# Optimization experiments

Measured on AMD Instinct MI355X. Metric: run time of the kernel, lower is better.

Reference implementation:

```python
import jax, jax.numpy as jnp
import numpy as np

N_HEADS = 16
ROPE_BASE = 10000.0


def _rope_cos_sin(seq_len, head_dim, dtype):
    half = head_dim // 2
    inv_freq = 1.0 / (ROPE_BASE ** (jnp.arange(0, half, dtype=jnp.float32) / half))
    ang = jnp.arange(seq_len, dtype=jnp.float32)[:, None] * inv_freq[None, :]  # [S, half]
    cos = jnp.concatenate([jnp.cos(ang), jnp.cos(ang)], axis=-1).astype(dtype)  # [S, hd]
    sin = jnp.concatenate([jnp.sin(ang), jnp.sin(ang)], axis=-1).astype(dtype)
    return cos, sin


def _rotate_half(x):
    half = x.shape[-1] // 2
    return jnp.concatenate([-x[..., half:], x[..., :half]], axis=-1)


def setup_inputs() -> dict:
    key = jax.random.key(0)
    k1, k2, k3 = jax.random.split(key, 3)
    B, S, D = 2, 2048, 1024
    x = jax.random.normal(k1, (B, S, D), dtype=jnp.float32)
    w_qkv = jax.random.normal(k2, (D, 3 * D), dtype=jnp.float32) * (1.0 / np.sqrt(D))
    w_out = jax.random.normal(k3, (D, D), dtype=jnp.float32) * (1.0 / np.sqrt(D))
    return {"x": x, "w_qkv": w_qkv, "w_out": w_out}


def reference(x, w_qkv, w_out):
    B, S, D = x.shape
    H = N_HEADS
    hd = D // H
    scale = 1.0 / np.sqrt(hd)

    qkv = x @ w_qkv  # [B, S, 3D]
    q, k, v = jnp.split(qkv, 3, axis=-1)
    # [B, H, S, hd]
    q = q.reshape(B, S, H, hd).transpose(0, 2, 1, 3)
    k = k.reshape(B, S, H, hd).transpose(0, 2, 1, 3)
    v = v.reshape(B, S, H, hd).transpose(0, 2, 1, 3)

    cos, sin = _rope_cos_sin(S, hd, x.dtype)  # [S, hd]
    q = q * cos + _rotate_half(q) * sin
    k = k * cos + _rotate_half(k) * sin

    scores = jnp.einsum("bhqd,bhkd->bhqk", q, k) * scale  # [B, H, S, S]
    causal = jnp.tril(jnp.ones((S, S), dtype=bool))
    scores = jnp.where(causal[None, None, :, :], scores, -jnp.inf)

    probs = jax.nn.softmax(scores.astype(jnp.float32), axis=-1).astype(q.dtype)
    out = jnp.einsum("bhqk,bhkd->bhqd", probs, v)  # [B, H, S, hd]
    out = out.transpose(0, 2, 1, 3).reshape(B, S, D)
    return out @ w_out
```

## Files before the change

### kernel.cpp

```cpp
#include <hip/hip_runtime.h>
#include <math.h>
#include <type_traits>

#define B_  2
#define S_  2048
#define D_  1024
#define H_  16

typedef short bf16x8 __attribute__((ext_vector_type(8)));
typedef short bf16x4 __attribute__((ext_vector_type(4)));
typedef float f32x4  __attribute__((ext_vector_type(4)));

__device__ __forceinline__ short f2bf(float f) {
    unsigned u = __builtin_bit_cast(unsigned, f);
    u += 0x7FFFu + ((u >> 16) & 1u);
    return (short)(u >> 16);
}
__device__ __forceinline__ float bf2f(short s) {
    unsigned u = ((unsigned)(unsigned short)s) << 16;
    return __builtin_bit_cast(float, u);
}

__device__ __forceinline__ void gload16(const short* g, const void* l) {
    __builtin_amdgcn_global_load_lds(
        (const __attribute__((address_space(1))) void*)g,
        (__attribute__((address_space(3))) void*)l, 16, 0, 0);
}

__device__ __forceinline__ void transpose_body(
    const float* __restrict__ in, short* __restrict__ out, int K, int N,
    int bx, int by, short (*t)[72], int tid)
{
    const int k0 = by * 64, n0 = bx * 64;
    const int r = tid >> 2;
    const int c = (tid & 3) * 16;
    const float* src = in + (size_t)(k0 + r) * N + n0 + c;
#pragma unroll
    for (int i = 0; i < 16; ++i) t[c + i][r] = f2bf(src[i]);
    __syncthreads();
    short* dst = out + (size_t)(n0 + r) * K + k0 + c;
    *(bf16x8*)(dst)     = *(const bf16x8*)&t[r][c];
    *(bf16x8*)(dst + 8) = *(const bf16x8*)&t[r][c + 8];
}

__global__ __launch_bounds__(256) void prep_kernel(
    const float* __restrict__ x, short* __restrict__ Xb,
    const float* __restrict__ w_qkv, short* __restrict__ Wqt,
    const float* __restrict__ w_out, short* __restrict__ Wot,
    float2* __restrict__ tab)
{
    __shared__ short t[64][72];
    const int bid = blockIdx.x;
    const int tid = threadIdx.x;
    if (bid < 2048) {
        int i = (bid * 256 + tid) * 8;
        float4 a = *(const float4*)(x + i);
        float4 b = *(const float4*)(x + i + 4);
        bf16x8 o;
        o[0] = f2bf(a.x); o[1] = f2bf(a.y); o[2] = f2bf(a.z); o[3] = f2bf(a.w);
        o[4] = f2bf(b.x); o[5] = f2bf(b.y); o[6] = f2bf(b.z); o[7] = f2bf(b.w);
        *(bf16x8*)(Xb + i) = o;
    } else if (bid < 2816) {
        int b2 = bid - 2048;
        transpose_body(w_qkv, Wqt, 1024, 3072, b2 % 48, b2 / 48, t, tid);
    } else if (bid < 3072) {
        int b2 = bid - 2816;
        transpose_body(w_out, Wot, 1024, 1024, b2 % 16, b2 / 16, t, tid);
    } else {
        int idx = (bid - 3072) * 256 + tid;
        int j = idx & 31, s = idx >> 5;
        float inv = powf(10000.0f, -(float)j * (1.0f / 32.0f));
        float sn, cs;
        sincosf((float)s * inv, &sn, &cs);
        tab[idx] = make_float2(cs, sn);
    }
}

__global__ __launch_bounds__(256) void gemm_bt_f32(
    const short* __restrict__ A, const short* __restrict__ Bt,
    float* __restrict__ C, int M, int N, int K)
{
    __shared__ short smem[18432];

    const int tid  = threadIdx.x;
    const int wave = tid >> 6, lane = tid & 63;
    const int quad = lane >> 4, l16 = lane & 15;
    const int wm = wave >> 1, wn = wave & 1;

    const int nbx = N >> 6;
    const int row0 = (blockIdx.x / nbx) * 128, col0 = (blockIdx.x % nbx) * 64;

    f32x4 acc[4][2];
#pragma unroll
    for (int mi = 0; mi < 4; ++mi)
#pragma unroll
        for (int ni = 0; ni < 2; ++ni) acc[mi][ni] = (f32x4)0.f;

    const int sr = tid >> 2;
    const int sc = (tid & 3) * 8;
    const short* a0 = A  + (size_t)(row0 + sr) * K + sc;
    const short* a1 = A  + (size_t)(row0 + 64 + sr) * K + sc;
    const short* b0 = Bt + (size_t)(col0 + sr) * K + sc;

    auto stage = [&](int b, int kt) {
        char* l = (char*)(smem + b * 6144) + wave * 1024;
        const int k0 = kt * 32;
        gload16(a0 + k0, l);
        gload16(a1 + k0, l + 4096);
        gload16(b0 + k0, l + 8192);
    };

    const int NT = K >> 5;
    stage(0, 0);
    stage(1, 1);
    int bufid = 0;
    for (int kt = 0; kt < NT; ++kt) {
        if (kt + 1 < NT) { asm volatile("s_waitcnt vmcnt(3)" ::: "memory"); }
        else             { asm volatile("s_waitcnt vmcnt(0)" ::: "memory"); }
        __builtin_amdgcn_s_barrier();
        __builtin_amdgcn_sched_barrier(0);
        if (kt + 2 < NT) {
            int nb = bufid + 2; if (nb >= 3) nb -= 3;
            stage(nb, kt + 2);
        }

        const short* As = smem + bufid * 6144;
        const short* Bs = As + 4096;
        bf16x8 af[4], bfr[2];
#pragma unroll
        for (int mi = 0; mi < 4; ++mi)
            af[mi] = *(const bf16x8*)(As + (wm * 64 + mi * 16 + l16) * 32 + quad * 8);
#pragma unroll
        for (int ni = 0; ni < 2; ++ni)
            bfr[ni] = *(const bf16x8*)(Bs + (wn * 32 + ni * 16 + l16) * 32 + quad * 8);
#pragma unroll
        for (int mi = 0; mi < 4; ++mi)
#pragma unroll
            for (int ni = 0; ni < 2; ++ni)
                acc[mi][ni] = __builtin_amdgcn_mfma_f32_16x16x32_bf16(
                    af[mi], bfr[ni], acc[mi][ni], 0, 0, 0);

        bufid = (bufid + 1 == 3) ? 0 : bufid + 1;
    }

#pragma unroll
    for (int mi = 0; mi < 4; ++mi)
#pragma unroll
        for (int ni = 0; ni < 2; ++ni)
#pragma unroll
            for (int r = 0; r < 4; ++r) {
                int row = row0 + wm * 64 + mi * 16 + quad * 4 + r;
                int col = col0 + wn * 32 + ni * 16 + l16;
                C[(size_t)row * N + col] = acc[mi][ni][r];
            }
}

__global__ __launch_bounds__(256) void gemm_qkv(
    const short* __restrict__ A, const short* __restrict__ Bt,
    const float2* __restrict__ tab,
    short* __restrict__ Qb, short* __restrict__ Kb, short* __restrict__ Vt)
{
    const int K = 1024;
    extern __shared__ short smem[];
    short* Sc = smem;

    const int tid  = threadIdx.x;
    const int wave = tid >> 6, lane = tid & 63;
    const int quad = lane >> 4, l16 = lane & 15;
    const int wm = wave >> 1, wn = wave & 1;

    const int row0 = (blockIdx.x / 24) * 128, col0 = (blockIdx.x % 24) * 128;

    f32x4 acc[4][4];
#pragma unroll
    for (int mi = 0; mi < 4; ++mi)
#pragma unroll
        for (int ni = 0; ni < 4; ++ni) acc[mi][ni] = (f32x4)0.f;

    const int sr = tid >> 2;
    const int sc = (tid & 3) * 8;
    const short* a0 = A  + (size_t)(row0 + sr) * K + sc;
    const short* a1 = A  + (size_t)(row0 + 64 + sr) * K + sc;
    const short* b0 = Bt + (size_t)(col0 + sr) * K + sc;
    const short* b1 = Bt + (size_t)(col0 + 64 + sr) * K + sc;

    auto stage = [&](int b, int kt) {
        char* l = (char*)(smem + b * 8192) + wave * 1024;
        const int k0 = kt * 32;
        gload16(a0 + k0, l);
        gload16(a1 + k0, l + 4096);
        gload16(b0 + k0, l + 8192);
        gload16(b1 + k0, l + 12288);
    };

    const int NT = K >> 5;
    stage(0, 0);
    stage(1, 1);
    int bufid = 0;
    for (int kt = 0; kt < NT; ++kt) {
        if (kt + 1 < NT) { asm volatile("s_waitcnt vmcnt(4)" ::: "memory"); }
        else             { asm volatile("s_waitcnt vmcnt(0)" ::: "memory"); }
        __builtin_amdgcn_s_barrier();
        __builtin_amdgcn_sched_barrier(0);
        if (kt + 2 < NT) {
            int nb = bufid + 2; if (nb >= 3) nb -= 3;
            stage(nb, kt + 2);
        }

        const short* As = smem + bufid * 8192;
        const short* Bs = As + 4096;
        bf16x8 af[4], bfr[4];
#pragma unroll
        for (int mi = 0; mi < 4; ++mi)
            af[mi] = *(const bf16x8*)(As + (wm * 64 + mi * 16 + l16) * 32 + quad * 8);
#pragma unroll
        for (int ni = 0; ni < 4; ++ni)
            bfr[ni] = *(const bf16x8*)(Bs + (wn * 64 + ni * 16 + l16) * 32 + quad * 8);
#pragma unroll
        for (int mi = 0; mi < 4; ++mi)
#pragma unroll
            for (int ni = 0; ni < 4; ++ni)
                acc[mi][ni] = __builtin_amdgcn_mfma_f32_16x16x32_bf16(
                    af[mi], bfr[ni], acc[mi][ni], 0, 0, 0);

        bufid = (bufid + 1 == 3) ? 0 : bufid + 1;
    }

    __syncthreads();

    const int sec  = (col0 + wn * 64) >> 6;
    const int h    = sec & 15;
    const int kind = sec >> 4;
    short* myS = Sc + wave * 4608;

    const int mrow0 = row0 + wm * 64;
    const int b  = mrow0 >> 11;
    const int bh = b * 16 + h;
    const int sbase = mrow0 & (S_ - 1);

    if (kind < 2) {
#pragma unroll
        for (int mi = 0; mi < 4; ++mi) {
#pragma unroll
            for (int r = 0; r < 4; ++r) {
                int sl = mi * 16 + quad * 4 + r;
                int s = sbase + sl;
#pragma unroll
                for (int ni = 0; ni < 2; ++ni) {
                    int j = ni * 16 + l16;
                    float2 t = tab[s * 32 + j];
                    float lo = acc[mi][ni][r], hi = acc[mi][ni + 2][r];
                    float olo = lo * t.x - hi * t.y;
                    float ohi = hi * t.x + lo * t.y;
                    if (kind == 0) { olo *= 0.125f; ohi *= 0.125f; }
                    myS[sl * 72 + j]      = f2bf(olo);
                    myS[sl * 72 + 32 + j] = f2bf(ohi);
                }
            }
        }
        const int rl = lane >> 3;
        const int cl = (lane & 7) * 8;
        short* dst = (kind == 0 ? Qb : Kb);
#pragma unroll
        for (int p = 0; p < 8; ++p) {
            int rr = p * 8 + rl;
            bf16x8 v = *(const bf16x8*)&myS[rr * 72 + cl];
            *(bf16x8*)(dst + ((size_t)bh * S_ + sbase + rr) * 64 + cl) = v;
        }
    } else {
#pragma unroll
        for (int mi = 0; mi < 4; ++mi)
#pragma unroll
            for (int ni = 0; ni < 4; ++ni) {
                bf16x4 p;
                p[0] = f2bf(acc[mi][ni][0]);
                p[1] = f2bf(acc[mi][ni][1]);
                p[2] = f2bf(acc[mi][ni][2]);
                p[3] = f2bf(acc[mi][ni][3]);
                *(bf16x4*)&myS[(ni * 16 + l16) * 72 + mi * 16 + quad * 4] = p;
            }
        const int rl = lane >> 3;
        const int cl = (lane & 7) * 8;
#pragma unroll
        for (int p = 0; p < 8; ++p) {
            int dd = p * 8 + rl;
            bf16x8 v = *(const bf16x8*)&myS[dd * 72 + cl];
            *(bf16x8*)(Vt + ((size_t)bh * 64 + dd) * S_ + sbase + cl) = v;
        }
    }
}

__global__ __launch_bounds__(256, 3) void attn_kernel(
    const short* __restrict__ Qb, const short* __restrict__ Kb,
    const short* __restrict__ Vt, short* __restrict__ Opart,
    float* __restrict__ lpart)
{
    __shared__ short Ks[2][64 * 64];
    __shared__ short Vs[2][64 * 64];
    __shared__ short Ps[128][72];

    const int lin = blockIdx.x;
    const int xcd = lin & 7;
    const int j   = lin >> 3;
    const int bh   = xcd * 4 + (j & 3);
    const int task = j >> 2;

    const int g = task < 4 ? 0 : task < 12 ? 1 : task < 24 ? 2 : 3;
    const int cumstart = g == 0 ? 0 : g == 1 ? 4 : g == 2 ? 12 : 24;
    const int idx = task - cumstart;
    const int qd = idx / (g + 1);
    const int qb = 4 * g + qd;
    const int c  = idx - qd * (g + 1);
    const int t0 = c * 8;
    const int t1 = min(2 * qb + 1, c * 8 + 7);

    const int wave = threadIdx.x >> 6, lane = threadIdx.x & 63;
    const int quad = lane >> 4, l16 = lane & 15;
    const int subr  = lane >> 3;
    const int chunk = (lane & 7) ^ subr;
    const size_t head64 = (size_t)bh * S_ * 64;

    bf16x8 qf[2][2];
#pragma unroll
    for (int m = 0; m < 2; ++m) {
        const short* qrow = Qb + head64
            + (size_t)(qb * 128 + wave * 32 + m * 16 + l16) * 64 + quad * 8;
        qf[m][0] = *(const bf16x8*)(qrow);
        qf[m][1] = *(const bf16x8*)(qrow + 32);
    }

    bf16x8 ones;
#pragma unroll
    for (int i = 0; i < 8; ++i) ones[i] = (short)0x3F80;

    auto stage = [&](int buf, int t) {
        const short* kt = Kb + head64 + (size_t)(t * 64 + wave * 16) * 64;
        const short* vt = Vt + head64 + (size_t)(wave * 16) * S_ + t * 64;
        char* kl = (char*)(Ks[buf]) + wave * 2048;
        char* vl = (char*)(Vs[buf]) + wave * 2048;
#pragma unroll
        for (int g2 = 0; g2 < 2; ++g2) {
            gload16(kt + (g2 * 8 + subr) * 64 + chunk * 8, kl + g2 * 1024);
            gload16(vt + (size_t)(g2 * 8 + subr) * S_ + chunk * 8, vl + g2 * 1024);
        }
    };

    f32x4 lacc[2] = {(f32x4)0.f, (f32x4)0.f};
    f32x4 oacc[2][4];
#pragma unroll
    for (int m = 0; m < 2; ++m)
#pragma unroll
        for (int nt = 0; nt < 4; ++nt) oacc[m][nt] = (f32x4)0.f;

    stage(0, t0);
    int buf = 0;
    for (int t = t0; t <= t1; ++t) {
        __builtin_amdgcn_s_barrier();
        if (t < t1) stage(buf ^ 1, t + 1);
        if (t < t1) { asm volatile("s_waitcnt vmcnt(4)" ::: "memory"); }
        else        { asm volatile("s_waitcnt vmcnt(0)" ::: "memory"); }
        __builtin_amdgcn_s_barrier();
        __builtin_amdgcn_sched_barrier(0);

        const short* kbuf = Ks[buf];
        const short* vbuf = Vs[buf];

        f32x4 s4[2][4];
        __builtin_amdgcn_s_setprio(1);
#pragma unroll
        for (int nt = 0; nt < 4; ++nt) {
            const int krow = nt * 16 + l16;
            const int sw = krow & 7;
            bf16x8 k0 = *(const bf16x8*)(kbuf + krow * 64 + ((quad ^ sw) << 3));
            bf16x8 k1 = *(const bf16x8*)(kbuf + krow * 64 + (((quad + 4) ^ sw) << 3));
#pragma unroll
            for (int m = 0; m < 2; ++m) {
                f32x4 a = (f32x4)0.f;
                a = __builtin_amdgcn_mfma_f32_16x16x32_bf16(k0, qf[m][0], a, 0, 0, 0);
                a = __builtin_amdgcn_mfma_f32_16x16x32_bf16(k1, qf[m][1], a, 0, 0, 0);
                s4[m][nt] = a;
            }
        }
        __builtin_amdgcn_s_setprio(0);

        if (t >= 2 * qb) {
            const int kbase = (t - 2 * qb) * 64;
#pragma unroll
            for (int m = 0; m < 2; ++m) {
                const int qq = wave * 32 + m * 16 + l16;
#pragma unroll
                for (int nt = 0; nt < 4; ++nt)
#pragma unroll
                    for (int r = 0; r < 4; ++r)
                        if (kbase + nt * 16 + quad * 4 + r > qq)
                            s4[m][nt][r] = -INFINITY;
            }
        }

#pragma unroll
        for (int m = 0; m < 2; ++m)
#pragma unroll
            for (int nt = 0; nt < 4; ++nt) {
                bf16x4 p;
#pragma unroll
                for (int r = 0; r < 4; ++r)
                    p[r] = f2bf(__expf(s4[m][nt][r] - 8.0f));
                *(bf16x4*)&Ps[wave * 32 + m * 16 + l16][nt * 16 + quad * 4] = p;
            }

        bf16x8 pa[2][2];
#pragma unroll
        for (int m = 0; m < 2; ++m) {
            pa[m][0] = *(const bf16x8*)&Ps[wave * 32 + m * 16 + l16][quad * 8];
            pa[m][1] = *(const bf16x8*)&Ps[wave * 32 + m * 16 + l16][32 + quad * 8];
        }

        __builtin_amdgcn_s_setprio(1);
#pragma unroll
        for (int m = 0; m < 2; ++m) {
            lacc[m] = __builtin_amdgcn_mfma_f32_16x16x32_bf16(pa[m][0], ones, lacc[m], 0, 0, 0);
            lacc[m] = __builtin_amdgcn_mfma_f32_16x16x32_bf16(pa[m][1], ones, lacc[m], 0, 0, 0);
        }
#pragma unroll
        for (int nt = 0; nt < 4; ++nt) {
            const int vrow = nt * 16 + l16;
            const int sw = vrow & 7;
            bf16x8 v0 = *(const bf16x8*)(vbuf + vrow * 64 + ((quad ^ sw) << 3));
            bf16x8 v1 = *(const bf16x8*)(vbuf + vrow * 64 + (((quad + 4) ^ sw) << 3));
#pragma unroll
            for (int m = 0; m < 2; ++m) {
                oacc[m][nt] = __builtin_amdgcn_mfma_f32_16x16x32_bf16(
                    pa[m][0], v0, oacc[m][nt], 0, 0, 0);
                oacc[m][nt] = __builtin_amdgcn_mfma_f32_16x16x32_bf16(
                    pa[m][1], v1, oacc[m][nt], 0, 0, 0);
            }
        }
        __builtin_amdgcn_s_setprio(0);
        buf ^= 1;
    }

    const int pidx = bh * 40 + task;
#pragma unroll
    for (int m = 0; m < 2; ++m)
#pragma unroll
        for (int r = 0; r < 4; ++r) {
            int ql = wave * 32 + m * 16 + quad * 4 + r;
            short* orow = Opart + (size_t)pidx * 8192 + ql * 64;
#pragma unroll
            for (int nt = 0; nt < 4; ++nt)
                orow[nt * 16 + l16] = f2bf(oacc[m][nt][r]);
            if (l16 == 0)
                lpart[(size_t)pidx * 128 + ql] = lacc[m][r];
        }
}

__global__ __launch_bounds__(256) void combine_kernel(
    const short* __restrict__ Opart, const float* __restrict__ lpart,
    short* __restrict__ attnb)
{
    const int qb = blockIdx.x, bh = blockIdx.y;
    const int g = qb >> 2, nch = g + 1;
    const int cumstart = g == 0 ? 0 : g == 1 ? 4 : g == 2 ? 12 : 24;
    const int cbase = bh * 40 + cumstart + (qb - 4 * g) * nch;
    const int q = threadIdx.x >> 1;
    const int dg = (threadIdx.x & 1) * 32;

    float lsum = 0.f;
    float acc[32];
#pragma unroll
    for (int i = 0; i < 32; ++i) acc[i] = 0.f;

    for (int cc = 0; cc < nch; ++cc) {
        lsum += lpart[(size_t)(cbase + cc) * 128 + q];
        const short* src = Opart + (size_t)(cbase + cc) * 8192 + q * 64 + dg;
#pragma unroll
        for (int w = 0; w < 4; ++w) {
            bf16x8 o = *(const bf16x8*)(src + w * 8);
#pragma unroll
            for (int i = 0; i < 8; ++i) acc[w * 8 + i] += bf2f(o[i]);
        }
    }
    float inv = 1.0f / lsum;
    const int b = bh >> 4, h = bh & 15;
    short* dst = attnb + (size_t)(b * S_ + qb * 128 + q) * 1024 + h * 64 + dg;
#pragma unroll
    for (int w = 0; w < 4; ++w) {
        bf16x8 r;
#pragma unroll
        for (int i = 0; i < 8; ++i) r[i] = f2bf(acc[w * 8 + i] * inv);
        *(bf16x8*)(dst + w * 8) = r;
    }
}

extern "C" void kernel_launch(void* const* d_in, const int* in_sizes, int n_in,
                              void* d_out, int out_size, void* d_ws, size_t ws_size,
                              hipStream_t stream)
{
    const float* x     = (const float*)d_in[0];
    const float* w_qkv = (const float*)d_in[1];
    const float* w_out = (const float*)d_in[2];
    float* out = (float*)d_out;

    short* Qb   = (short*)d_ws;
    short* Kb   = Qb   + (size_t)4096 * 1024;
    short* Vt   = Kb   + (size_t)4096 * 1024;
    short* Xb   = Vt   + (size_t)4096 * 1024;
    short* Wqt  = Xb   + (size_t)4096 * 1024;
    short* Wot  = Wqt  + (size_t)3072 * 1024;
    float2* tab = (float2*)(Wot + (size_t)1024 * 1024);
    short* Opart = (short*)(tab + 2048 * 32);
    float* lbuf  = (float*)(Opart + (size_t)1280 * 8192);
    short* attnb = Xb;

    prep_kernel<<<3328, 256, 0, stream>>>(x, Xb, w_qkv, Wqt, w_out, Wot, tab);

    gemm_qkv<<<768, 256, 49152, stream>>>(Xb, Wqt, tab, Qb, Kb, Vt);

    attn_kernel<<<1280, 256, 0, stream>>>(Qb, Kb, Vt, Opart, lbuf);

    combine_kernel<<<dim3(16, 32), 256, 0, stream>>>(Opart, lbuf, attnb);

    gemm_bt_f32<<<512, 256, 0, stream>>>(attnb, Wot, out, 4096, 1024, 1024);
}
```

Measured before the change: 174.1 us.

## Double attention query tile to 256 rows per block to reuse K/V loads

Each attention block now handles 256 query rows (two 128-row halves processed in sequence) instead of 128, so every staged K/V tile feeds twice as many query rows. This halves the grid to 640 blocks and changes the split-K chunk schedule and the partial buffer layout, with the combine kernel updated to match. The cost is more live registers (double Q fragments and accumulators) under the same launch bounds, possible spills or lower occupancy, and fewer blocks available to balance the causal workload.

New measurement: 204.4 us. 17.4% more time.

```diff
diff --git a/kernel.cpp b/kernel.cpp
--- a/kernel.cpp
+++ b/kernel.cpp
@@ -305,14 +305,17 @@
     const int bh   = xcd * 4 + (j & 3);
     const int task = j >> 2;
 
-    const int g = task < 4 ? 0 : task < 12 ? 1 : task < 24 ? 2 : 3;
-    const int cumstart = g == 0 ? 0 : g == 1 ? 4 : g == 2 ? 12 : 24;
-    const int idx = task - cumstart;
-    const int qd = idx / (g + 1);
-    const int qb = 4 * g + qd;
-    const int c  = idx - qd * (g + 1);
+    int qb, c;
+    if      (task < 1)  { qb = 0; c = task;      }
+    else if (task < 2)  { qb = 1; c = task - 1;  }
+    else if (task < 4)  { qb = 2; c = task - 2;  }
+    else if (task < 6)  { qb = 3; c = task - 4;  }
+    else if (task < 9)  { qb = 4; c = task - 6;  }
+    else if (task < 12) { qb = 5; c = task - 9;  }
+    else if (task < 16) { qb = 6; c = task - 12; }
+    else                { qb = 7; c = task - 16; }
     const int t0 = c * 8;
-    const int t1 = min(2 * qb + 1, c * 8 + 7);
+    const int t1 = min(4 * qb + 3, c * 8 + 7);
 
     const int wave = threadIdx.x >> 6, lane = threadIdx.x & 63;
     const int quad = lane >> 4, l16 = lane & 15;
@@ -320,13 +323,14 @@
     const int chunk = (lane & 7) ^ subr;
     const size_t head64 = (size_t)bh * S_ * 64;
 
-    bf16x8 qf[2][2];
-#pragma unroll
-    for (int m = 0; m < 2; ++m) {
+    bf16x8 qf[4][2];
+#pragma unroll
+    for (int cc = 0; cc < 4; ++cc) {
+        const int row = (cc >> 1) * 128 + wave * 32 + (cc & 1) * 16 + l16;
         const short* qrow = Qb + head64
-            + (size_t)(qb * 128 + wave * 32 + m * 16 + l16) * 64 + quad * 8;
-        qf[m][0] = *(const bf16x8*)(qrow);
-        qf[m][1] = *(const bf16x8*)(qrow + 32);
+            + (size_t)(qb * 256 + row) * 64 + quad * 8;
+        qf[cc][0] = *(const bf16x8*)(qrow);
+        qf[cc][1] = *(const bf16x8*)(qrow + 32);
     }
 
     bf16x8 ones;
@@ -345,12 +349,12 @@
         }
     };
 
-    f32x4 lacc[2] = {(f32x4)0.f, (f32x4)0.f};
-    f32x4 oacc[2][4];
-#pragma unroll
-    for (int m = 0; m < 2; ++m)
-#pragma unroll
-        for (int nt = 0; nt < 4; ++nt) oacc[m][nt] = (f32x4)0.f;
+    f32x4 lacc[4] = {(f32x4)0.f, (f32x4)0.f, (f32x4)0.f, (f32x4)0.f};
+    f32x4 oacc[4][4];
+#pragma unroll
+    for (int cc = 0; cc < 4; ++cc)
+#pragma unroll
+        for (int nt = 0; nt < 4; ++nt) oacc[cc][nt] = (f32x4)0.f;
 
     stage(0, t0);
     int buf = 0;
@@ -364,93 +368,101 @@
 
         const short* kbuf = Ks[buf];
         const short* vbuf = Vs[buf];
-
-        f32x4 s4[2][4];
-        __builtin_amdgcn_s_setprio(1);
-#pragma unroll
-        for (int nt = 0; nt < 4; ++nt) {
-            const int krow = nt * 16 + l16;
-            const int sw = krow & 7;
-            bf16x8 k0 = *(const bf16x8*)(kbuf + krow * 64 + ((quad ^ sw) << 3));
-            bf16x8 k1 = *(const bf16x8*)(kbuf + krow * 64 + (((quad + 4) ^ sw) << 3));
+        const int diag = t - 4 * qb;
+
+#pragma unroll
+        for (int mm = 0; mm < 2; ++mm) {
+            f32x4 s4[2][4];
+            __builtin_amdgcn_s_setprio(1);
+#pragma unroll
+            for (int nt = 0; nt < 4; ++nt) {
+                const int krow = nt * 16 + l16;
+                const int sw = krow & 7;
+                bf16x8 k0 = *(const bf16x8*)(kbuf + krow * 64 + ((quad ^ sw) << 3));
+                bf16x8 k1 = *(const bf16x8*)(kbuf + krow * 64 + (((quad + 4) ^ sw) << 3));
+#pragma unroll
+                for (int m = 0; m < 2; ++m) {
+                    f32x4 a = (f32x4)0.f;
+                    a = __builtin_amdgcn_mfma_f32_16x16x32_bf16(
+                        k0, qf[mm * 2 + m][0], a, 0, 0, 0);
+                    a = __builtin_amdgcn_mfma_f32_16x16x32_bf16(
+                        k1, qf[mm * 2 + m][1], a, 0, 0, 0);
+                    s4[m][nt] = a;
+                }
+            }
+            __builtin_amdgcn_s_setprio(0);
+
+            if (diag >= 0) {
+                const int kbase = diag * 64;
+#pragma unroll
+                for (int m = 0; m < 2; ++m) {
+                    const int qq = mm * 128 + wave * 32 + m * 16 + l16;
+#pragma unroll
+                    for (int nt = 0; nt < 4; ++nt)
+#pragma unroll
+                        for (int r = 0; r < 4; ++r)
+                            if (kbase + nt * 16 + quad * 4 + r > qq)
+                                s4[m][nt][r] = -INFINITY;
+                }
+            }
+
+#pragma unroll
+            for (int m = 0; m < 2; ++m)
+#pragma unroll
+                for (int nt = 0; nt < 4; ++nt) {
+                    bf16x4 p;
+#pragma unroll
+                    for (int r = 0; r < 4; ++r)
+                        p[r] = f2bf(__expf(s4[m][nt][r] - 8.0f));
+                    *(bf16x4*)&Ps[wave * 32 + m * 16 + l16][nt * 16 + quad * 4] = p;
+                }
+
+            bf16x8 pa[2][2];
 #pragma unroll
             for (int m = 0; m < 2; ++m) {
-                f32x4 a = (f32x4)0.f;
-                a = __builtin_amdgcn_mfma_f32_16x16x32_bf16(k0, qf[m][0], a, 0, 0, 0);
-                a = __builtin_amdgcn_mfma_f32_16x16x32_bf16(k1, qf[m][1], a, 0, 0, 0);
-                s4[m][nt] = a;
-            }
-        }
-        __builtin_amdgcn_s_setprio(0);
-
-        if (t >= 2 * qb) {
-            const int kbase = (t - 2 * qb) * 64;
+                pa[m][0] = *(const bf16x8*)&Ps[wave * 32 + m * 16 + l16][quad * 8];
+                pa[m][1] = *(const bf16x8*)&Ps[wave * 32 + m * 16 + l16][32 + quad * 8];
+            }
+
+            __builtin_amdgcn_s_setprio(1);
 #pragma unroll
             for (int m = 0; m < 2; ++m) {
-                const int qq = wave * 32 + m * 16 + l16;
-#pragma unroll
-                for (int nt = 0; nt < 4; ++nt)
-#pragma unroll
-                    for (int r = 0; r < 4; ++r)
-                        if (kbase + nt * 16 + quad * 4 + r > qq)
-                            s4[m][nt][r] = -INFINITY;
-            }
-        }
-
-#pragma unroll
-        for (int m = 0; m < 2; ++m)
+                lacc[mm * 2 + m] = __builtin_amdgcn_mfma_f32_16x16x32_bf16(
+                    pa[m][0], ones, lacc[mm * 2 + m], 0, 0, 0);
+                lacc[mm * 2 + m] = __builtin_amdgcn_mfma_f32_16x16x32_bf16(
+                    pa[m][1], ones, lacc[mm * 2 + m], 0, 0, 0);
+            }
 #pragma unroll
             for (int nt = 0; nt < 4; ++nt) {
-                bf16x4 p;
-#pragma unroll
-                for (int r = 0; r < 4; ++r)
-                    p[r] = f2bf(__expf(s4[m][nt][r] - 8.0f));
-                *(bf16x4*)&Ps[wave * 32 + m * 16 + l16][nt * 16 + quad * 4] = p;
-            }
-
-        bf16x8 pa[2][2];
-#pragma unroll
-        for (int m = 0; m < 2; ++m) {
-            pa[m][0] = *(const bf16x8*)&Ps[wave * 32 + m * 16 + l16][quad * 8];
-            pa[m][1] = *(const bf16x8*)&Ps[wave * 32 + m * 16 + l16][32 + quad * 8];
-        }
-
-        __builtin_amdgcn_s_setprio(1);
-#pragma unroll
-        for (int m = 0; m < 2; ++m) {
-            lacc[m] = __builtin_amdgcn_mfma_f32_16x16x32_bf16(pa[m][0], ones, lacc[m], 0, 0, 0);
-            lacc[m] = __builtin_amdgcn_mfma_f32_16x16x32_bf16(pa[m][1], ones, lacc[m], 0, 0, 0);
-        }
-#pragma unroll
-        for (int nt = 0; nt < 4; ++nt) {
-            const int vrow = nt * 16 + l16;
-            const int sw = vrow & 7;
-            bf16x8 v0 = *(const bf16x8*)(vbuf + vrow * 64 + ((quad ^ sw) << 3));
-            bf16x8 v1 = *(const bf16x8*)(vbuf + vrow * 64 + (((quad + 4) ^ sw) << 3));
-#pragma unroll
-            for (int m = 0; m < 2; ++m) {
-                oacc[m][nt] = __builtin_amdgcn_mfma_f32_16x16x32_bf16(
-                    pa[m][0], v0, oacc[m][nt], 0, 0, 0);
-                oacc[m][nt] = __builtin_amdgcn_mfma_f32_16x16x32_bf16(
-                    pa[m][1], v1, oacc[m][nt], 0, 0, 0);
-            }
-        }
-        __builtin_amdgcn_s_setprio(0);
+                const int vrow = nt * 16 + l16;
+                const int sw = vrow & 7;
+                bf16x8 v0 = *(const bf16x8*)(vbuf + vrow * 64 + ((quad ^ sw) << 3));
+                bf16x8 v1 = *(const bf16x8*)(vbuf + vrow * 64 + (((quad + 4) ^ sw) << 3));
+#pragma unroll
+                for (int m = 0; m < 2; ++m) {
+                    oacc[mm * 2 + m][nt] = __builtin_amdgcn_mfma_f32_16x16x32_bf16(
+                        pa[m][0], v0, oacc[mm * 2 + m][nt], 0, 0, 0);
+                    oacc[mm * 2 + m][nt] = __builtin_amdgcn_mfma_f32_16x16x32_bf16(
+                        pa[m][1], v1, oacc[mm * 2 + m][nt], 0, 0, 0);
+                }
+            }
+            __builtin_amdgcn_s_setprio(0);
+        }
         buf ^= 1;
     }
 
-    const int pidx = bh * 40 + task;
-#pragma unroll
-    for (int m = 0; m < 2; ++m)
+    const int pidx = bh * 20 + task;
+#pragma unroll
+    for (int cc = 0; cc < 4; ++cc)
 #pragma unroll
         for (int r = 0; r < 4; ++r) {
-            int ql = wave * 32 + m * 16 + quad * 4 + r;
-            short* orow = Opart + (size_t)pidx * 8192 + ql * 64;
+            int ql = (cc >> 1) * 128 + wave * 32 + (cc & 1) * 16 + quad * 4 + r;
+            short* orow = Opart + (size_t)pidx * 16384 + ql * 64;
 #pragma unroll
             for (int nt = 0; nt < 4; ++nt)
-                orow[nt * 16 + l16] = f2bf(oacc[m][nt][r]);
+                orow[nt * 16 + l16] = f2bf(oacc[cc][nt][r]);
             if (l16 == 0)
-                lpart[(size_t)pidx * 128 + ql] = lacc[m][r];
+                lpart[(size_t)pidx * 256 + ql] = lacc[cc][r];
         }
 }
 
@@ -458,11 +470,12 @@
     const short* __restrict__ Opart, const float* __restrict__ lpart,
     short* __restrict__ attnb)
 {
-    const int qb = blockIdx.x, bh = blockIdx.y;
-    const int g = qb >> 2, nch = g + 1;
-    const int cumstart = g == 0 ? 0 : g == 1 ? 4 : g == 2 ? 12 : 24;
-    const int cbase = bh * 40 + cumstart + (qb - 4 * g) * nch;
-    const int q = threadIdx.x >> 1;
+    const int hb = blockIdx.x, bh = blockIdx.y;
+    const int qb = hb >> 1, rbase = (hb & 1) * 128;
+    const int nch = (qb + 2) >> 1;
+    const int cumt[8] = {0, 1, 2, 4, 6, 9, 12, 16};
+    const int cbase = bh * 20 + cumt[qb];
+    const int q = rbase + (threadIdx.x >> 1);
     const int dg = (threadIdx.x & 1) * 32;
 
     float lsum = 0.f;
@@ -471,8 +484,8 @@
     for (int i = 0; i < 32; ++i) acc[i] = 0.f;
 
     for (int cc = 0; cc < nch; ++cc) {
-        lsum += lpart[(size_t)(cbase + cc) * 128 + q];
-        const short* src = Opart + (size_t)(cbase + cc) * 8192 + q * 64 + dg;
+        lsum += lpart[(size_t)(cbase + cc) * 256 + q];
+        const short* src = Opart + (size_t)(cbase + cc) * 16384 + q * 64 + dg;
 #pragma unroll
         for (int w = 0; w < 4; ++w) {
             bf16x8 o = *(const bf16x8*)(src + w * 8);
@@ -482,7 +495,7 @@
     }
     float inv = 1.0f / lsum;
     const int b = bh >> 4, h = bh & 15;
-    short* dst = attnb + (size_t)(b * S_ + qb * 128 + q) * 1024 + h * 64 + dg;
+    short* dst = attnb + (size_t)(b * S_ + qb * 256 + q) * 1024 + h * 64 + dg;
 #pragma unroll
     for (int w = 0; w < 4; ++w) {
         bf16x8 r;
@@ -509,14 +522,14 @@
     short* Wot  = Wqt  + (size_t)3072 * 1024;
     float2* tab = (float2*)(Wot + (size_t)1024 * 1024);
     short* Opart = (short*)(tab + 2048 * 32);
-    float* lbuf  = (float*)(Opart + (size_t)1280 * 8192);
+    float* lbuf  = (float*)(Opart + (size_t)640 * 16384);
     short* attnb = Xb;
 
     prep_kernel<<<3328, 256, 0, stream>>>(x, Xb, w_qkv, Wqt, w_out, Wot, tab);
 
     gemm_qkv<<<768, 256, 49152, stream>>>(Xb, Wqt, tab, Qb, Kb, Vt);
 
-    attn_kernel<<<1280, 256, 0, stream>>>(Qb, Kb, Vt, Opart, lbuf);
+    attn_kernel<<<640, 256, 0, stream>>>(Qb, Kb, Vt, Opart, lbuf);
 
     combine_kernel<<<dim3(16, 32), 256, 0, stream>>>(Opart, lbuf, attnb);
 
```
